# Performance work log

Measured on AMD Instinct MI355X. Metric: run time of the kernel, lower is better.

## Reference

```python
import jax, jax.numpy as jnp
import numpy as np

N, E, D = 100000, 1600000, 128


def setup_inputs() -> dict:
    key = jax.random.key(0)
    ks = jax.random.split(key, 8)
    s = 1.0 / np.sqrt(D)
    return {
        "x": jax.random.normal(ks[0], (N, D), dtype=jnp.float32),
        "edge_index": jax.random.randint(ks[1], (2, E), 0, N, dtype=jnp.int64),
        "x_prev": jax.random.normal(ks[2], (N, D), dtype=jnp.float32),
        # GCNConv params: weight [in,out], bias [out]
        "W": jax.random.uniform(ks[3], (D, D), jnp.float32, -s, s),
        "b": jnp.zeros((D,), jnp.float32),
        # GRUCell params (torch layout): [3*H, H] gates ordered (r, z, n)
        "W_ih": jax.random.uniform(ks[4], (3 * D, D), jnp.float32, -s, s),
        "W_hh": jax.random.uniform(ks[5], (3 * D, D), jnp.float32, -s, s),
        "b_ih": jax.random.uniform(ks[6], (3 * D,), jnp.float32, -s, s),
        "b_hh": jax.random.uniform(ks[7], (3 * D,), jnp.float32, -s, s),
    }


def _gcn_conv(x, edge_index, W, b):
    n = x.shape[0]
    loop = jnp.arange(n, dtype=edge_index.dtype)
    src = jnp.concatenate([edge_index[0], loop])  # [E+N]
    dst = jnp.concatenate([edge_index[1], loop])
    # symmetric normalization: deg over destinations (incl. self loops)
    deg = jax.ops.segment_sum(jnp.ones_like(dst, dtype=x.dtype), dst, num_segments=n)
    dinv = jnp.where(deg > 0, jax.lax.rsqrt(deg), 0.0)
    norm = dinv[src] * dinv[dst]  # [E+N]
    xw = x @ W  # [N, out]
    msg = xw[src] * norm[:, None]  # gather + scale
    return jax.ops.segment_sum(msg, dst, num_segments=n) + b


def _gru_cell(inp, h, W_ih, W_hh, b_ih, b_hh):
    gi = inp @ W_ih.T + b_ih  # [N, 3H]
    gh = h @ W_hh.T + b_hh
    i_r, i_z, i_n = jnp.split(gi, 3, axis=-1)
    h_r, h_z, h_n = jnp.split(gh, 3, axis=-1)
    r = jax.nn.sigmoid(i_r + h_r)
    z = jax.nn.sigmoid(i_z + h_z)
    ntil = jnp.tanh(i_n + r * h_n)
    return (1.0 - z) * ntil + z * h


def reference(x, edge_index, x_prev, W, b, W_ih, W_hh, b_ih, b_hh):
    h_cur = _gcn_conv(x, edge_index, W, b)
    return _gru_cell(h_cur, x_prev, W_ih, W_hh, b_ih, b_hh)
```

## Files before the change

kernel.cpp:

```cpp
#include <hip/hip_runtime.h>
#include <hip/hip_bf16.h>
#include <math.h>

#define DIM 128
#define PSHIFT 10
#define PSZ 1024
#define CHUNK 4096

typedef __attribute__((ext_vector_type(8))) short bf16x8;
typedef __attribute__((ext_vector_type(4))) float f32x4;
typedef __attribute__((ext_vector_type(2))) float f32x2;
typedef unsigned short u16;
typedef unsigned char u8;
typedef unsigned int u32;
typedef unsigned long long u64;

__device__ __forceinline__ u16 f2bf(float x) {
    u32 u = __builtin_bit_cast(u32, x);
    u += 0x7fff + ((u >> 16) & 1);
    return (u16)(u >> 16);
}
__device__ __forceinline__ float bf2f(u16 h) {
    return __builtin_bit_cast(float, (u32)h << 16);
}
__device__ __forceinline__ float fsig(float x) {
    return __builtin_amdgcn_rcpf(1.f + __expf(-x));
}
__device__ __forceinline__ float ftanh(float x) {
    return 1.f - 2.f * __builtin_amdgcn_rcpf(__expf(2.f * x) + 1.f);
}
__device__ __forceinline__ u8 f2fp8(float v) {
    int pk = __builtin_amdgcn_cvt_pk_fp8_f32(v, v, 0, false);
    return (u8)(pk & 0xff);
}


__global__ __launch_bounds__(256) void k_zero(int* __restrict__ p, int n) {
    int i = blockIdx.x * 256 + threadIdx.x;
    if (i < n) p[i] = 0;
}

__global__ __launch_bounds__(256) void k_pcount(const int* __restrict__ edst,
                                                int* __restrict__ pcnt, int E) {
    __shared__ int h[128];
    int t = threadIdx.x;
    if (t < 128) h[t] = 0;
    __syncthreads();
    int stride = gridDim.x * 256;
    for (int e = blockIdx.x * 256 + t; e < E; e += stride)
        atomicAdd(&h[edst[e] >> PSHIFT], 1);
    __syncthreads();
    if (t < 128 && h[t]) atomicAdd(&pcnt[t], h[t]);
}

__global__ __launch_bounds__(256) void k_pscan(const int* __restrict__ pcnt,
                                               int* __restrict__ poff,
                                               int* __restrict__ pfill,
                                               int* __restrict__ rowp,
                                               int P, int N, int E) {
    __shared__ int a[256];
    int t = threadIdx.x;
    int v = (t < P) ? pcnt[t] : 0;
    a[t] = v;
    __syncthreads();
    #pragma unroll
    for (int off = 1; off < 256; off <<= 1) {
        int y = (t >= off) ? a[t - off] : 0;
        __syncthreads();
        a[t] += y;
        __syncthreads();
    }
    int excl = a[t] - v;
    if (t < P) { poff[t] = excl; pfill[t] = excl; }
    if (t == 0) { poff[P] = E; rowp[N] = E; }
}

__global__ __launch_bounds__(256) void k_pscatter(const int* __restrict__ esrc,
                                                  const int* __restrict__ edst,
                                                  int* __restrict__ pfill,
                                                  u64* __restrict__ pbuf, int E) {
    __shared__ int hist[128], sc[128], lofs[128], gbase[128];
    __shared__ u32 ss[CHUNK], sd[CHUNK];
    int t = threadIdx.x;
    int c0 = blockIdx.x * CHUNK;
    int cnt = E - c0; if (cnt > CHUNK) cnt = CHUNK;

    if (t < 128) hist[t] = 0;
    __syncthreads();

    u32 s[16], d[16];
    int p[16], r[16];
    #pragma unroll
    for (int j = 0; j < 16; ++j) {
        int i = j * 256 + t;
        if (i < cnt) {
            s[j] = (u32)esrc[c0 + i];
            d[j] = (u32)edst[c0 + i];
            p[j] = (int)(d[j] >> PSHIFT);
            r[j] = atomicAdd(&hist[p[j]], 1);
        }
    }
    __syncthreads();

    if (t < 128) sc[t] = hist[t];
    __syncthreads();
    #pragma unroll
    for (int off = 1; off < 128; off <<= 1) {
        int y = 0;
        if (t < 128 && t >= off) y = sc[t - off];
        __syncthreads();
        if (t < 128) sc[t] += y;
        __syncthreads();
    }
    if (t < 128) {
        lofs[t] = sc[t] - hist[t];
        if (hist[t] > 0) gbase[t] = atomicAdd(&pfill[t], hist[t]);
    }
    __syncthreads();

    #pragma unroll
    for (int j = 0; j < 16; ++j) {
        int i = j * 256 + t;
        if (i < cnt) {
            int idx = lofs[p[j]] + r[j];
            ss[idx] = s[j];
            sd[idx] = d[j];
        }
    }
    __syncthreads();

    for (int i = t; i < cnt; i += 256) {
        u32 dd = sd[i];
        int pp = (int)(dd >> PSHIFT);
        int gpos = gbase[pp] + (i - lofs[pp]);
        pbuf[gpos] = (u64)ss[i] | ((u64)dd << 32);
    }
}

__global__ __launch_bounds__(256) void k_pfill(const u64* __restrict__ pbuf,
                                               const int* __restrict__ poff,
                                               int* __restrict__ rowp,
                                               int* __restrict__ srcs,
                                               float* __restrict__ dinv, int N) {
    __shared__ int cnt[PSZ];
    __shared__ int wsum[4];
    int p = blockIdx.x, t = threadIdx.x;
    int lane = t & 63, wid = t >> 6;
    int nb0 = p << PSHIFT;
    int ncnt = N - nb0; if (ncnt > PSZ) ncnt = PSZ;
    int b0 = poff[p], b1 = poff[p + 1];
    int bc = b1 - b0;

    for (int i = t; i < PSZ; i += 256) cnt[i] = 0;
    __syncthreads();
    for (int i = t; i < bc; i += 256) {
        u32 d = (u32)(pbuf[b0 + i] >> 32);
        atomicAdd(&cnt[d - nb0], 1);
    }
    __syncthreads();

    int base = t * 4;
    int c[4];
    int ssum = 0;
    #pragma unroll
    for (int j = 0; j < 4; ++j) { c[j] = cnt[base + j]; ssum += c[j]; }
    int incl = ssum;
    #pragma unroll
    for (int off = 1; off < 64; off <<= 1) {
        int y = __shfl_up(incl, off, 64);
        if (lane >= off) incl += y;
    }
    if (lane == 63) wsum[wid] = incl;
    __syncthreads();
    int add = 0;
    for (int w = 0; w < wid; ++w) add += wsum[w];
    int rr = b0 + add + (incl - ssum);
    #pragma unroll
    for (int j = 0; j < 4; ++j) {
        int i = base + j;
        if (i < ncnt) {
            rowp[nb0 + i] = rr;
            dinv[nb0 + i] = rsqrtf((float)(c[j] + 1));
        }
        cnt[i] = rr;
        rr += c[j];
    }
    __syncthreads();

    for (int i = t; i < bc; i += 256) {
        u64 v = pbuf[b0 + i];
        u32 sv = (u32)v;
        u32 d = (u32)(v >> 32);
        int pos = atomicAdd(&cnt[d - nb0], 1);
        srcs[pos] = (int)sv;
    }
}


__global__ __launch_bounds__(256) void k_prep(const float* __restrict__ W,
                                              const float* __restrict__ Wih,
                                              const float* __restrict__ Whh,
                                              const float4* __restrict__ xp,
                                              u16* __restrict__ Wt,
                                              u16* __restrict__ Wihb,
                                              u16* __restrict__ Whhb,
                                              u32* __restrict__ Xpb, int n4) {
    int gid = blockIdx.x * 256 + threadIdx.x;
    int stride = gridDim.x * 256;
    for (int i = gid; i < n4; i += stride) {
        float4 v = xp[i];
        Xpb[i * 2 + 0] = (u32)f2bf(v.x) | ((u32)f2bf(v.y) << 16);
        Xpb[i * 2 + 1] = (u32)f2bf(v.z) | ((u32)f2bf(v.w) << 16);
    }
    if (gid < 128 * 128) {
        int k = gid >> 7, c = gid & 127;
        Wt[c * 128 + k] = f2bf(W[gid]);
    }
    if (gid < 3 * 128 * 128) {
        Wihb[gid] = f2bf(Wih[gid]);
        Whhb[gid] = f2bf(Whh[gid]);
    }
}


__global__ __launch_bounds__(256) void k_gemm1(const float* __restrict__ X,
                                               const u16* __restrict__ Wt,
                                               const float* __restrict__ dinv,
                                               u8* __restrict__ XW8, int n) {
    __shared__ u16 Wlds[128 * 128];
    int t = threadIdx.x, w = t >> 6, l = t & 63;
    int lr = l & 15, q = l >> 4;

    for (int cidx = t; cidx < 2048; cidx += 256) {
        int r = cidx >> 4, kc = cidx & 15;
        int dst = r * 128 + ((kc * 8) ^ ((r & 7) << 3));
        *(bf16x8*)(Wlds + dst) = *(const bf16x8*)(Wt + r * 128 + kc * 8);
    }
    __syncthreads();

    int r0 = blockIdx.x * 128;
    int wrow0 = r0 + w * 32;
    int sw = (lr & 7) << 3;
    int ar0 = wrow0 + lr;      if (ar0 > n - 1) ar0 = n - 1;
    int ar1 = wrow0 + 16 + lr; if (ar1 > n - 1) ar1 = n - 1;
    const float* x0 = X + (size_t)ar0 * DIM;
    const float* x1 = X + (size_t)ar1 * DIM;

    f32x4 acc[2][8];
    #pragma unroll
    for (int s = 0; s < 2; ++s)
        #pragma unroll
        for (int c = 0; c < 8; ++c) acc[s][c] = (f32x4){0.f, 0.f, 0.f, 0.f};

    #pragma unroll
    for (int kb = 0; kb < 4; ++kb) {
        int ko = kb * 32 + q * 8;
        float4 f00 = *(const float4*)(x0 + ko), f01 = *(const float4*)(x0 + ko + 4);
        float4 f10 = *(const float4*)(x1 + ko), f11 = *(const float4*)(x1 + ko + 4);
        bf16x8 a0, a1;
        a0[0] = (short)f2bf(f00.x); a0[1] = (short)f2bf(f00.y);
        a0[2] = (short)f2bf(f00.z); a0[3] = (short)f2bf(f00.w);
        a0[4] = (short)f2bf(f01.x); a0[5] = (short)f2bf(f01.y);
        a0[6] = (short)f2bf(f01.z); a0[7] = (short)f2bf(f01.w);
        a1[0] = (short)f2bf(f10.x); a1[1] = (short)f2bf(f10.y);
        a1[2] = (short)f2bf(f10.z); a1[3] = (short)f2bf(f10.w);
        a1[4] = (short)f2bf(f11.x); a1[5] = (short)f2bf(f11.y);
        a1[6] = (short)f2bf(f11.z); a1[7] = (short)f2bf(f11.w);
        int kw = ko ^ sw;
        #pragma unroll
        for (int ct = 0; ct < 8; ++ct) {
            bf16x8 b = *(const bf16x8*)(Wlds + (ct * 16 + lr) * 128 + kw);
            acc[0][ct] = __builtin_amdgcn_mfma_f32_16x16x32_bf16(a0, b, acc[0][ct], 0, 0, 0);
            acc[1][ct] = __builtin_amdgcn_mfma_f32_16x16x32_bf16(a1, b, acc[1][ct], 0, 0, 0);
        }
    }

    float dv[2][4];
    #pragma unroll
    for (int s = 0; s < 2; ++s)
        #pragma unroll
        for (int i = 0; i < 4; ++i) {
            int row = wrow0 + s * 16 + q * 4 + i; if (row > n - 1) row = n - 1;
            dv[s][i] = dinv[row];
        }
    #pragma unroll
    for (int s = 0; s < 2; ++s)
        #pragma unroll
        for (int ct = 0; ct < 8; ++ct)
            #pragma unroll
            for (int i = 0; i < 4; ++i) {
                int row = wrow0 + s * 16 + q * 4 + i;
                if (row < n)
                    XW8[(size_t)row * DIM + ct * 16 + lr] = f2fp8(acc[s][ct][i] * dv[s][i]);
            }
}


__global__ __launch_bounds__(256) void k_gather(const u8* __restrict__ XW8,
                                                const float* __restrict__ dinv,
                                                const int* __restrict__ row_ptr,
                                                const int* __restrict__ srcs,
                                                const float* __restrict__ bias,
                                                u16* __restrict__ Hcb, int n) {
    int node = blockIdx.x * 4 + (threadIdx.x >> 6);
    if (node >= n) return;
    int lane = threadIdx.x & 63;
    int c = lane * 2;

    u16 sv = *(const u16*)(XW8 + (size_t)node * DIM + c);
    f32x2 sf = __builtin_amdgcn_cvt_pk_f32_fp8((int)(u32)sv, false);
    float accx = sf[0], accy = sf[1];

    int e = row_ptr[node], end = row_ptr[node + 1];
    for (; e + 7 < end; e += 8) {
        int sdx[8]; u16 vv[8];
        #pragma unroll
        for (int j = 0; j < 8; ++j) sdx[j] = srcs[e + j];
        #pragma unroll
        for (int j = 0; j < 8; ++j)
            vv[j] = *(const u16*)(XW8 + (size_t)sdx[j] * DIM + c);
        #pragma unroll
        for (int j = 0; j < 8; ++j) {
            f32x2 f = __builtin_amdgcn_cvt_pk_f32_fp8((int)(u32)vv[j], false);
            accx += f[0];
            accy += f[1];
        }
    }
    for (; e < end; ++e) {
        u16 v = *(const u16*)(XW8 + (size_t)srcs[e] * DIM + c);
        f32x2 f = __builtin_amdgcn_cvt_pk_f32_fp8((int)(u32)v, false);
        accx += f[0];
        accy += f[1];
    }
    float di = dinv[node];
    float ox = accx * di + bias[c];
    float oy = accy * di + bias[c + 1];
    *(u32*)(Hcb + (size_t)node * DIM + c) = (u32)f2bf(ox) | ((u32)f2bf(oy) << 16);
}


__global__ __launch_bounds__(256) void k_gru(const u16* __restrict__ Hcb,
                                             const u16* __restrict__ Xpb,
                                             const u16* __restrict__ Wihb,
                                             const u16* __restrict__ Whhb,
                                             const float* __restrict__ bih,
                                             const float* __restrict__ bhh,
                                             float* __restrict__ Out, int n) {
    int t = threadIdx.x, w = t >> 6, l = t & 63;
    int lr = l & 15, q = l >> 4;

    int nwg = gridDim.x;
    int qq = nwg >> 3, rr8 = nwg & 7;
    int xcd = blockIdx.x & 7, idx = blockIdx.x >> 3;
    int logical = (xcd < rr8 ? xcd * (qq + 1) : rr8 * (qq + 1) + (xcd - rr8) * qq) + idx;
    int cs = logical & 7;
    int slot = logical >> 3;
    int nslot = nwg >> 3;
    int c0 = cs * 16;

    bf16x8 bI[4][3], bH[4][3];
    #pragma unroll
    for (int kb = 0; kb < 4; ++kb)
        #pragma unroll
        for (int g = 0; g < 3; ++g) {
            size_t off = (size_t)(g * 128 + c0 + lr) * DIM + kb * 32 + q * 8;
            bI[kb][g] = *(const bf16x8*)(Wihb + off);
            bH[kb][g] = *(const bf16x8*)(Whhb + off);
        }

    int j = c0 + lr;
    float br = bih[j],       bz = bih[128 + j], bn = bih[256 + j];
    float cr = bhh[j],       cz = bhh[128 + j], cn = bhh[256 + j];

    int nrb = (n + 63) >> 6;
    for (int rb = slot; rb < nrb; rb += nslot) {
        int wrow0 = rb * 64 + w * 16;
        int ar = wrow0 + lr; if (ar > n - 1) ar = n - 1;
        const u16* hb = Hcb + (size_t)ar * DIM;
        const u16* xb = Xpb + (size_t)ar * DIM;

        u16 hp16[4];
        #pragma unroll
        for (int i = 0; i < 4; ++i) {
            int row = wrow0 + q * 4 + i; if (row > n - 1) row = n - 1;
            hp16[i] = Xpb[(size_t)row * DIM + j];
        }

        f32x4 aI[3], aH[3];
        #pragma unroll
        for (int g = 0; g < 3; ++g) {
            aI[g] = (f32x4){0.f, 0.f, 0.f, 0.f};
            aH[g] = (f32x4){0.f, 0.f, 0.f, 0.f};
        }

        #pragma unroll
        for (int kb = 0; kb < 4; ++kb) {
            int ko = kb * 32 + q * 8;
            bf16x8 hA = *(const bf16x8*)(hb + ko);
            bf16x8 xA = *(const bf16x8*)(xb + ko);
            #pragma unroll
            for (int g = 0; g < 3; ++g) {
                aI[g] = __builtin_amdgcn_mfma_f32_16x16x32_bf16(hA, bI[kb][g], aI[g], 0, 0, 0);
                aH[g] = __builtin_amdgcn_mfma_f32_16x16x32_bf16(xA, bH[kb][g], aH[g], 0, 0, 0);
            }
        }

        #pragma unroll
        for (int i = 0; i < 4; ++i) {
            int row = wrow0 + q * 4 + i;
            if (row >= n) continue;
            float ir = aI[0][i] + br;
            float iz = aI[1][i] + bz;
            float in_ = aI[2][i] + bn;
            float hr = aH[0][i] + cr;
            float hz = aH[1][i] + cz;
            float hn = aH[2][i] + cn;
            float rg = fsig(ir + hr);
            float zg = fsig(iz + hz);
            float ng = ftanh(in_ + rg * hn);
            float hp = bf2f(hp16[i]);
            Out[(size_t)row * DIM + j] = (1.f - zg) * ng + zg * hp;
        }
    }
}


extern "C" void kernel_launch(void* const* d_in, const int* in_sizes, int n_in,
                              void* d_out, int out_size, void* d_ws, size_t ws_size,
                              hipStream_t stream) {
    const float* x     = (const float*)d_in[0];
    const int*   ei    = (const int*)d_in[1];
    const float* xprev = (const float*)d_in[2];
    const float* W     = (const float*)d_in[3];
    const float* b     = (const float*)d_in[4];
    const float* Wih   = (const float*)d_in[5];
    const float* Whh   = (const float*)d_in[6];
    const float* bih   = (const float*)d_in[7];
    const float* bhh   = (const float*)d_in[8];

    int N = in_sizes[0] / DIM;
    int E = in_sizes[1] / 2;
    int P = (N + PSZ - 1) >> PSHIFT;
    const int* esrc = ei;
    const int* edst = ei + E;

    char* p = (char*)d_ws;
    auto alloc = [&](size_t bytes) {
        char* q = p;
        p += (bytes + 255) & ~(size_t)255;
        return q;
    };
    float* dinv = (float*)alloc((size_t)N * 4);
    int*   rowp = (int*)  alloc((size_t)(N + 1) * 4);
    int*   srcs = (int*)  alloc((size_t)E * 4);
    u16*   Hcb  = (u16*)  alloc((size_t)N * DIM * 2);
    u16*   Xpb  = (u16*)  alloc((size_t)N * DIM * 2);
    size_t xwsz = (size_t)N * DIM;
    size_t pbsz = (size_t)E * 8;
    u8*    XW8  = (u8*)   alloc(xwsz > pbsz ? xwsz : pbsz);
    u16*   Wt   = (u16*)  alloc(128 * 128 * 2);
    u16*   Wihb = (u16*)  alloc(3 * 128 * 128 * 2);
    u16*   Whhb = (u16*)  alloc(3 * 128 * 128 * 2);
    int*   pcnt = (int*)  alloc(128 * 4);
    int*   poff = (int*)  alloc(129 * 4);
    int*   pfil = (int*)  alloc(128 * 4);
    u64*   pbuf = (u64*)XW8;
    float* out  = (float*)d_out;

    k_zero    <<<1, 256, 0, stream>>>(pcnt, 128);
    k_pcount  <<<1024, 256, 0, stream>>>(edst, pcnt, E);
    k_pscan   <<<1, 256, 0, stream>>>(pcnt, poff, pfil, rowp, P, N, E);
    int nch = (E + CHUNK - 1) / CHUNK;
    k_pscatter<<<nch, 256, 0, stream>>>(esrc, edst, pfil, pbuf, E);
    k_pfill   <<<P, 256, 0, stream>>>(pbuf, poff, rowp, srcs, dinv, N);
    int n4 = N * DIM / 4;
    k_prep    <<<2048, 256, 0, stream>>>(W, Wih, Whh, (const float4*)xprev,
                                         Wt, Wihb, Whhb, (u32*)Xpb, n4);
    int nrb = (N + 127) / 128;
    k_gemm1   <<<nrb, 256, 0, stream>>>(x, Wt, dinv, XW8, N);
    k_gather  <<<(N + 3) / 4, 256, 0, stream>>>(XW8, dinv, rowp, srcs, b, Hcb, N);
    k_gru     <<<1536, 256, 0, stream>>>(Hcb, Xpb, Wihb, Whhb, bih, bhh, out, N);
}
```

Before: 273.2 us.

## Restage GRU weights in LDS with 1024-thread blocks and fuse prep into edge count

The GRU kernel now uses 256 blocks of 1024 threads. Each block stages half of the W_ih/W_hh columns (96 KB) into swizzled LDS once, so weights are no longer held in registers, and each block processes two row chunks per iteration with their loads issued up front. The bf16 conversion prep kernel is merged into the partition-count kernel, and the zeroing kernel is replaced by a memset, cutting launches. The GRU update is rewritten as an fma. The risks are lower occupancy from the large LDS footprint, LDS read pressure on every MFMA, and the count kernel now doing extra streaming work.

Result: slower. 407.1 us (+49.0%).

```diff
diff --git a/kernel.cpp b/kernel.cpp
--- a/kernel.cpp
+++ b/kernel.cpp
@@ -35,20 +35,37 @@
 }
 
 
-__global__ __launch_bounds__(256) void k_zero(int* __restrict__ p, int n) {
-    int i = blockIdx.x * 256 + threadIdx.x;
-    if (i < n) p[i] = 0;
-}
-
-__global__ __launch_bounds__(256) void k_pcount(const int* __restrict__ edst,
-                                                int* __restrict__ pcnt, int E) {
+__global__ __launch_bounds__(256) void k_prepcount(const int* __restrict__ edst,
+                                                   int* __restrict__ pcnt, int E,
+                                                   const float* __restrict__ W,
+                                                   const float* __restrict__ Wih,
+                                                   const float* __restrict__ Whh,
+                                                   const float4* __restrict__ xp,
+                                                   u16* __restrict__ Wt,
+                                                   u16* __restrict__ Wihb,
+                                                   u16* __restrict__ Whhb,
+                                                   u32* __restrict__ Xpb, int n4) {
     __shared__ int h[128];
     int t = threadIdx.x;
+    int gid = blockIdx.x * 256 + t;
+    int stride = gridDim.x * 256;
     if (t < 128) h[t] = 0;
     __syncthreads();
-    int stride = gridDim.x * 256;
-    for (int e = blockIdx.x * 256 + t; e < E; e += stride)
+    for (int e = gid; e < E; e += stride)
         atomicAdd(&h[edst[e] >> PSHIFT], 1);
+    for (int i = gid; i < n4; i += stride) {
+        float4 v = xp[i];
+        Xpb[i * 2 + 0] = (u32)f2bf(v.x) | ((u32)f2bf(v.y) << 16);
+        Xpb[i * 2 + 1] = (u32)f2bf(v.z) | ((u32)f2bf(v.w) << 16);
+    }
+    if (gid < 128 * 128) {
+        int k = gid >> 7, c = gid & 127;
+        Wt[c * 128 + k] = f2bf(W[gid]);
+    }
+    if (gid < 3 * 128 * 128) {
+        Wihb[gid] = f2bf(Wih[gid]);
+        Whhb[gid] = f2bf(Whh[gid]);
+    }
     __syncthreads();
     if (t < 128 && h[t]) atomicAdd(&pcnt[t], h[t]);
 }
@@ -193,32 +210,6 @@
         u32 d = (u32)(v >> 32);
         int pos = atomicAdd(&cnt[d - nb0], 1);
         srcs[pos] = (int)sv;
-    }
-}
-
-
-__global__ __launch_bounds__(256) void k_prep(const float* __restrict__ W,
-                                              const float* __restrict__ Wih,
-                                              const float* __restrict__ Whh,
-                                              const float4* __restrict__ xp,
-                                              u16* __restrict__ Wt,
-                                              u16* __restrict__ Wihb,
-                                              u16* __restrict__ Whhb,
-                                              u32* __restrict__ Xpb, int n4) {
-    int gid = blockIdx.x * 256 + threadIdx.x;
-    int stride = gridDim.x * 256;
-    for (int i = gid; i < n4; i += stride) {
-        float4 v = xp[i];
-        Xpb[i * 2 + 0] = (u32)f2bf(v.x) | ((u32)f2bf(v.y) << 16);
-        Xpb[i * 2 + 1] = (u32)f2bf(v.z) | ((u32)f2bf(v.w) << 16);
-    }
-    if (gid < 128 * 128) {
-        int k = gid >> 7, c = gid & 127;
-        Wt[c * 128 + k] = f2bf(W[gid]);
-    }
-    if (gid < 3 * 128 * 128) {
-        Wihb[gid] = f2bf(Wih[gid]);
-        Whhb[gid] = f2bf(Whh[gid]);
     }
 }
 
@@ -339,75 +330,63 @@
 }
 
 
-__global__ __launch_bounds__(256) void k_gru(const u16* __restrict__ Hcb,
-                                             const u16* __restrict__ Xpb,
-                                             const u16* __restrict__ Wihb,
-                                             const u16* __restrict__ Whhb,
-                                             const float* __restrict__ bih,
-                                             const float* __restrict__ bhh,
-                                             float* __restrict__ Out, int n) {
+__global__ __launch_bounds__(1024) void k_gru(const u16* __restrict__ Hcb,
+                                              const u16* __restrict__ Xpb,
+                                              const u16* __restrict__ Wihb,
+                                              const u16* __restrict__ Whhb,
+                                              const float* __restrict__ bih,
+                                              const float* __restrict__ bhh,
+                                              float* __restrict__ Out, int n) {
+    __shared__ u16 Wlds[384 * 128];
     int t = threadIdx.x, w = t >> 6, l = t & 63;
     int lr = l & 15, q = l >> 4;
-
-    int nwg = gridDim.x;
-    int qq = nwg >> 3, rr8 = nwg & 7;
-    int xcd = blockIdx.x & 7, idx = blockIdx.x >> 3;
-    int logical = (xcd < rr8 ? xcd * (qq + 1) : rr8 * (qq + 1) + (xcd - rr8) * qq) + idx;
-    int cs = logical & 7;
-    int slot = logical >> 3;
-    int nslot = nwg >> 3;
-    int c0 = cs * 16;
-
-    bf16x8 bI[4][3], bH[4][3];
-    #pragma unroll
-    for (int kb = 0; kb < 4; ++kb)
-        #pragma unroll
-        for (int g = 0; g < 3; ++g) {
-            size_t off = (size_t)(g * 128 + c0 + lr) * DIM + kb * 32 + q * 8;
-            bI[kb][g] = *(const bf16x8*)(Wihb + off);
-            bH[kb][g] = *(const bf16x8*)(Whhb + off);
-        }
-
-    int j = c0 + lr;
-    float br = bih[j],       bz = bih[128 + j], bn = bih[256 + j];
-    float cr = bhh[j],       cz = bhh[128 + j], cn = bhh[256 + j];
-
-    int nrb = (n + 63) >> 6;
-    for (int rb = slot; rb < nrb; rb += nslot) {
-        int wrow0 = rb * 64 + w * 16;
-        int ar = wrow0 + lr; if (ar > n - 1) ar = n - 1;
-        const u16* hb = Hcb + (size_t)ar * DIM;
-        const u16* xb = Xpb + (size_t)ar * DIM;
-
-        u16 hp16[4];
-        #pragma unroll
-        for (int i = 0; i < 4; ++i) {
-            int row = wrow0 + q * 4 + i; if (row > n - 1) row = n - 1;
-            hp16[i] = Xpb[(size_t)row * DIM + j];
-        }
-
+    int bid = blockIdx.x;
+    int xcd = bid & 7, slot = bid >> 3;
+    int ch = slot & 1;
+    int rp = xcd * 16 + (slot >> 1);
+    int cs = w & 3, rg = w >> 2;
+    int csl = cs * 16;
+
+    for (int idx = t; idx < 6144; idx += 1024) {
+        int r = idx >> 4, kc = idx & 15;
+        int m = (r >= 192);
+        int rr = m ? r - 192 : r;
+        int g = rr >> 6, cc = rr & 63;
+        const u16* src = (m ? Whhb : Wihb)
+                       + (size_t)((g << 7) + ch * 64 + cc) * DIM + kc * 8;
+        int dst = r * 128 + ((kc * 8) ^ ((r & 7) << 3));
+        *(bf16x8*)(Wlds + dst) = *(const bf16x8*)src;
+    }
+    __syncthreads();
+
+    int sw = (lr & 7) << 3;
+    int jj = ch * 64 + csl + lr;
+    float br = bih[jj],       bz = bih[128 + jj], bn = bih[256 + jj];
+    float cr = bhh[jj],       cz = bhh[128 + jj], cn = bhh[256 + jj];
+
+    auto compute = [&](int r0, const bf16x8* hA, const bf16x8* xA,
+                       const u16* hp16) {
         f32x4 aI[3], aH[3];
         #pragma unroll
         for (int g = 0; g < 3; ++g) {
             aI[g] = (f32x4){0.f, 0.f, 0.f, 0.f};
             aH[g] = (f32x4){0.f, 0.f, 0.f, 0.f};
         }
-
         #pragma unroll
         for (int kb = 0; kb < 4; ++kb) {
-            int ko = kb * 32 + q * 8;
-            bf16x8 hA = *(const bf16x8*)(hb + ko);
-            bf16x8 xA = *(const bf16x8*)(xb + ko);
+            int kw = (kb * 32 + q * 8) ^ sw;
             #pragma unroll
             for (int g = 0; g < 3; ++g) {
-                aI[g] = __builtin_amdgcn_mfma_f32_16x16x32_bf16(hA, bI[kb][g], aI[g], 0, 0, 0);
-                aH[g] = __builtin_amdgcn_mfma_f32_16x16x32_bf16(xA, bH[kb][g], aH[g], 0, 0, 0);
+                int ridx = (g * 64 + csl + lr) * 128 + kw;
+                bf16x8 bI = *(const bf16x8*)(Wlds + ridx);
+                bf16x8 bH = *(const bf16x8*)(Wlds + ridx + 192 * 128);
+                aI[g] = __builtin_amdgcn_mfma_f32_16x16x32_bf16(hA[kb], bI, aI[g], 0, 0, 0);
+                aH[g] = __builtin_amdgcn_mfma_f32_16x16x32_bf16(xA[kb], bH, aH[g], 0, 0, 0);
             }
         }
-
         #pragma unroll
         for (int i = 0; i < 4; ++i) {
-            int row = wrow0 + q * 4 + i;
+            int row = r0 + q * 4 + i;
             if (row >= n) continue;
             float ir = aI[0][i] + br;
             float iz = aI[1][i] + bz;
@@ -415,12 +394,55 @@
             float hr = aH[0][i] + cr;
             float hz = aH[1][i] + cz;
             float hn = aH[2][i] + cn;
-            float rg = fsig(ir + hr);
-            float zg = fsig(iz + hz);
-            float ng = ftanh(in_ + rg * hn);
-            float hp = bf2f(hp16[i]);
-            Out[(size_t)row * DIM + j] = (1.f - zg) * ng + zg * hp;
-        }
+            float rg_ = fsig(ir + hr);
+            float zc  = fsig(-(iz + hz));
+            float ng  = ftanh(in_ + rg_ * hn);
+            float hp  = bf2f(hp16[i]);
+            Out[(size_t)row * DIM + jj] = fmaf(zc, ng - hp, hp);
+        }
+    };
+
+    int C = (n + 63) >> 6;
+    for (int c = rp; c < C; c += 256) {
+        int c2 = c + 128;
+        bool do2 = (c2 < C);
+
+        int r0a = c * 64 + rg * 16;
+        int ara = r0a + lr; if (ara > n - 1) ara = n - 1;
+        const u16* hba = Hcb + (size_t)ara * DIM;
+        const u16* xba = Xpb + (size_t)ara * DIM;
+        bf16x8 hA[4], xA[4]; u16 hpa[4];
+        #pragma unroll
+        for (int kb = 0; kb < 4; ++kb) {
+            hA[kb] = *(const bf16x8*)(hba + kb * 32 + q * 8);
+            xA[kb] = *(const bf16x8*)(xba + kb * 32 + q * 8);
+        }
+        #pragma unroll
+        for (int i = 0; i < 4; ++i) {
+            int row = r0a + q * 4 + i; if (row > n - 1) row = n - 1;
+            hpa[i] = Xpb[(size_t)row * DIM + jj];
+        }
+
+        int r0b = c2 * 64 + rg * 16;
+        bf16x8 hB[4], xB[4]; u16 hpb[4];
+        if (do2) {
+            int arb = r0b + lr; if (arb > n - 1) arb = n - 1;
+            const u16* hbb = Hcb + (size_t)arb * DIM;
+            const u16* xbb = Xpb + (size_t)arb * DIM;
+            #pragma unroll
+            for (int kb = 0; kb < 4; ++kb) {
+                hB[kb] = *(const bf16x8*)(hbb + kb * 32 + q * 8);
+                xB[kb] = *(const bf16x8*)(xbb + kb * 32 + q * 8);
+            }
+            #pragma unroll
+            for (int i = 0; i < 4; ++i) {
+                int row = r0b + q * 4 + i; if (row > n - 1) row = n - 1;
+                hpb[i] = Xpb[(size_t)row * DIM + jj];
+            }
+        }
+
+        compute(r0a, hA, xA, hpa);
+        if (do2) compute(r0b, hB, xB, hpb);
     }
 }
 
@@ -467,17 +489,17 @@
     u64*   pbuf = (u64*)XW8;
     float* out  = (float*)d_out;
 
-    k_zero    <<<1, 256, 0, stream>>>(pcnt, 128);
-    k_pcount  <<<1024, 256, 0, stream>>>(edst, pcnt, E);
+    hipMemsetAsync(pcnt, 0, 128 * 4, stream);
+    int n4 = N * DIM / 4;
+    k_prepcount<<<2048, 256, 0, stream>>>(edst, pcnt, E, W, Wih, Whh,
+                                          (const float4*)xprev,
+                                          Wt, Wihb, Whhb, (u32*)Xpb, n4);
     k_pscan   <<<1, 256, 0, stream>>>(pcnt, poff, pfil, rowp, P, N, E);
     int nch = (E + CHUNK - 1) / CHUNK;
     k_pscatter<<<nch, 256, 0, stream>>>(esrc, edst, pfil, pbuf, E);
     k_pfill   <<<P, 256, 0, stream>>>(pbuf, poff, rowp, srcs, dinv, N);
-    int n4 = N * DIM / 4;
-    k_prep    <<<2048, 256, 0, stream>>>(W, Wih, Whh, (const float4*)xprev,
-                                         Wt, Wihb, Whhb, (u32*)Xpb, n4);
     int nrb = (N + 127) / 128;
     k_gemm1   <<<nrb, 256, 0, stream>>>(x, Wt, dinv, XW8, N);
     k_gather  <<<(N + 3) / 4, 256, 0, stream>>>(XW8, dinv, rowp, srcs, b, Hcb, N);
-    k_gru     <<<1536, 256, 0, stream>>>(Hcb, Xpb, Wihb, Whhb, bih, bhh, out, N);
-}
+    k_gru     <<<256, 1024, 0, stream>>>(Hcb, Xpb, Wihb, Whhb, bih, bhh, out, N);
+}
```
